# Kernel tuning notes

Measured on AMD Instinct MI355X. Metric: run time of the kernel, lower is better.

Reference implementation:

```python
import jax, jax.numpy as jnp
import numpy as np

T, B, C, H = 2048, 2, 1024, 16
DK = C // H


def setup_inputs() -> dict:
    key = jax.random.key(0)
    ks = jax.random.split(key, 12)
    s = 1.0 / np.sqrt(C)
    return {
        "query": jax.random.normal(ks[0], (T, B, C), jnp.float32),
        "key": jax.random.normal(ks[1], (T, B, C), jnp.float32),
        "value": jax.random.normal(ks[2], (T, B, C), jnp.float32),
        "Wq": jax.random.normal(ks[3], (C, C), jnp.float32) * s,
        "bq": jnp.zeros((C,), jnp.float32),
        "Wk": jax.random.normal(ks[4], (C, C), jnp.float32) * s,
        "bk": jnp.zeros((C,), jnp.float32),
        "Wv": jax.random.normal(ks[5], (C, C), jnp.float32) * s,
        "bv": jnp.zeros((C,), jnp.float32),
        "Wo": jax.random.normal(ks[6], (C, C), jnp.float32) * s,
        "bo": jnp.zeros((C,), jnp.float32),
        "key_padding_mask": jax.random.randint(ks[7], (B, T), 0, 2).astype(jnp.bool_),
    }


def reference(query, key, value, Wq, bq, Wk, bk, Wv, bv, Wo, bo, key_padding_mask):
    # T,B,C -> B,T,C
    q_in = jnp.transpose(query, (1, 0, 2))
    k_in = jnp.transpose(key, (1, 0, 2))
    v_in = jnp.transpose(value, (1, 0, 2))
    nb = q_in.shape[0]
    # linear projections, split heads: B,T,C -> B,H,T,dk
    def proj(x, W, b):
        y = x @ W.T + b
        return jnp.transpose(y.reshape(nb, -1, H, DK), (0, 2, 1, 3))
    q = proj(q_in, Wq, bq)
    k = proj(k_in, Wk, bk)
    v = proj(v_in, Wv, bv)
    # scores: B,H,T1,T2
    scores = jnp.einsum("bhqd,bhkd->bhqk", q, k) / np.sqrt(DK).astype(np.float32)
    scores = jnp.where(key_padding_mask[:, None, None, :], -jnp.inf, scores)
    attn = jax.nn.softmax(scores, axis=-1)
    # context: B,H,T1,dk -> B,T1,C
    x = jnp.einsum("bhqk,bhkd->bhqd", attn, v)
    x = jnp.transpose(x, (0, 2, 1, 3)).reshape(nb, -1, H * DK)
    out = x @ Wo.T + bo
    # B,T,C -> T,B,C
    return jnp.transpose(out, (1, 0, 2))
```

## Files before the change

### kernel.cpp

```cpp
#include <hip/hip_runtime.h>
#include <stdint.h>

typedef __attribute__((ext_vector_type(4))) float f32x4;
typedef __attribute__((ext_vector_type(8))) short bf16x8;
typedef __attribute__((ext_vector_type(2))) unsigned int u32x2;
typedef unsigned short u16;
typedef unsigned int u32;

#define DEVINL __device__ __forceinline__

DEVINL u16 f2bf(float f) {
  u32 u = __builtin_bit_cast(u32, f);
  u += 0x7FFFu + ((u >> 16) & 1u);
  return (u16)(u >> 16);
}

DEVINL float exp2_hw(float x) {
  float r;
  asm("v_exp_f32 %0, %1\n\ts_nop 0" : "=v"(r) : "v"(x));
  return r;
}

DEVINL u32 cvt_pk_bf16(float lo, float hi) {
  u32 r;
  asm("v_cvt_pk_bf16_f32 %0, %1, %2" : "=v"(r) : "v"(lo), "v"(hi));
  return r;
}

DEVINL void gload16(const void* g, void* l) {
  __builtin_amdgcn_global_load_lds((const __attribute__((address_space(1))) void*)g,
                                   (__attribute__((address_space(3))) void*)l, 16, 0, 0);
}

__global__ void cvt_all(const float* __restrict__ q, const float* __restrict__ k,
                        const float* __restrict__ v, const float* __restrict__ wq,
                        const float* __restrict__ wk, const float* __restrict__ wv,
                        const float* __restrict__ wo, ushort4* __restrict__ dst) {
  int i = blockIdx.x * 256 + threadIdx.x;
  float4 v4;
  if (i < 1048576) v4 = ((const float4*)q)[i];
  else if (i < 2097152) v4 = ((const float4*)k)[i - 1048576];
  else if (i < 3145728) v4 = ((const float4*)v)[i - 2097152];
  else {
    int j = i - 3145728;
    if (j < 262144) v4 = ((const float4*)wq)[j];
    else if (j < 524288) v4 = ((const float4*)wk)[j - 262144];
    else if (j < 786432) v4 = ((const float4*)wv)[j - 524288];
    else v4 = ((const float4*)wo)[j - 786432];
  }
  ushort4 o;
  o.x = f2bf(v4.x); o.y = f2bf(v4.y); o.z = f2bf(v4.z); o.w = f2bf(v4.w);
  dst[i] = o;
}

__global__ void mask_prep(const u32* __restrict__ mraw, float* __restrict__ mout) {
  __shared__ int notint, notfloat;
  int tid = threadIdx.x;
  if (tid == 0) { notint = 0; notfloat = 0; }
  __syncthreads();
  u32 w = mraw[tid];
  if (w != 0u && w != 1u) notint = 1;
  if (w != 0u && w != 0x3f800000u) notfloat = 1;
  __syncthreads();
  bool words = (!notint) || (!notfloat);
  for (int i = tid; i < 4096; i += 1024) {
    u32 v = words ? mraw[i] : (u32)(((const unsigned char*)mraw)[i]);
    mout[i] = v ? -1.0e38f : 0.0f;
  }
}

DEVINL void gemm_body(const u16* __restrict__ A, const u16* __restrict__ W,
                      const float* __restrict__ bias, u16* __restrict__ out_bf,
                      float* __restrict__ out_f, int tile, int mode,
                      u16* As, u16* Bs) {
  const int tid = threadIdx.x, lane = tid & 63;
  const int wave = tid >> 6, wm = wave & 1, wn = wave >> 1;
  const int m0 = (tile >> 3) << 7;
  const int n0 = (tile & 7) << 7;
  const int l15 = lane & 15, l4 = lane >> 4;
  const int K = 1024;
  const f32x4 zero = {0.f, 0.f, 0.f, 0.f};
  f32x4 acc[4][4];
#pragma unroll
  for (int i = 0; i < 4; i++)
#pragma unroll
    for (int j = 0; j < 4; j++) acc[i][j] = zero;

  for (int kt = 0; kt < 1024; kt += 32) {
#pragma unroll
    for (int it = 0; it < 2; ++it) {
      int c = tid + (it << 8);
      int row = c >> 2, qs = (c & 3) ^ ((row & 3) ^ ((row >> 2) & 3));
      gload16(A + (size_t)(m0 + row) * K + kt + qs * 8, (void*)(As + c * 8));
      gload16(W + (size_t)(n0 + row) * K + kt + qs * 8, (void*)(Bs + c * 8));
    }
    __syncthreads();
    bf16x8 af[4], bfr[4];
#pragma unroll
    for (int i = 0; i < 4; i++) {
      int ra = (wm << 6) + (i << 4) + l15;
      int rb = (wn << 6) + (i << 4) + l15;
      af[i]  = *(const bf16x8*)(As + ra * 32 + ((l4 * 8) ^ ((((ra & 3) ^ ((ra >> 2) & 3))) << 3)));
      bfr[i] = *(const bf16x8*)(Bs + rb * 32 + ((l4 * 8) ^ ((((rb & 3) ^ ((rb >> 2) & 3))) << 3)));
    }
#pragma unroll
    for (int i = 0; i < 4; i++)
#pragma unroll
      for (int j = 0; j < 4; j++)
        acc[i][j] = __builtin_amdgcn_mfma_f32_16x16x32_bf16(af[i], bfr[j], acc[i][j], 0, 0, 0);
    __syncthreads();
  }

#pragma unroll
  for (int j = 0; j < 4; j++) {
    const int col = n0 + (wn << 6) + (j << 4) + l15;
    const float bc = bias[col];
#pragma unroll
    for (int i = 0; i < 4; i++) {
#pragma unroll
      for (int r = 0; r < 4; r++) {
        const int row = m0 + (wm << 6) + (i << 4) + (l4 << 2) + r;
        float v = acc[i][j][r] + bc;
        if (mode == 3) {
          int t = row & 2047, b2 = row >> 11;
          out_f[(size_t)(t * 2 + b2) * 1024 + col] = v;
        } else {
          int t = row >> 1, b2 = row & 1, h = col >> 6, dh = col & 63;
          if (mode == 2)
            out_bf[((size_t)(b2 * 16 + h) * 64 + dh) * 2048 + t] = f2bf(v);
          else
            out_bf[((size_t)(b2 * 16 + h) * 2048 + t) * 64 + dh] = f2bf(v);
        }
      }
    }
  }
}

__global__ __launch_bounds__(256, 3) void gemm_qkv(
    const u16* __restrict__ qbf, const u16* __restrict__ kbf, const u16* __restrict__ vbf,
    const u16* __restrict__ wq, const u16* __restrict__ wk, const u16* __restrict__ wv,
    const float* __restrict__ bq, const float* __restrict__ bk, const float* __restrict__ bv,
    u16* __restrict__ Qh, u16* __restrict__ Kh, u16* __restrict__ Vth) {
  __shared__ u16 As[4096], Bs[4096];
  int wg = blockIdx.x;
  int swz = (wg & 7) * 96 + (wg >> 3);
  int prob = swz >> 8, tile = swz & 255;
  if (prob == 0)      gemm_body(qbf, wq, bq, Qh,  nullptr, tile, 0, As, Bs);
  else if (prob == 1) gemm_body(kbf, wk, bk, Kh,  nullptr, tile, 0, As, Bs);
  else                gemm_body(vbf, wv, bv, Vth, nullptr, tile, 2, As, Bs);
}

__global__ __launch_bounds__(256, 3) void gemm_o(
    const u16* __restrict__ ctx, const u16* __restrict__ wo,
    const float* __restrict__ bo, float* __restrict__ out) {
  __shared__ u16 As[4096], Bs[4096];
  int wg = blockIdx.x;
  int swz = (wg & 7) * 32 + (wg >> 3);
  gemm_body(ctx, wo, bo, nullptr, out, swz, 3, As, Bs);
}

__global__ __launch_bounds__(256, 4) void attn_fwd(
    const u16* __restrict__ Qh, const u16* __restrict__ Kh, const u16* __restrict__ Vt,
    const float* __restrict__ maskf, u16* __restrict__ ctx) {
  __shared__ u16 Ks[2][64 * 64];
  __shared__ u16 Vs[2][64 * 64];
  __shared__ u32 Plu[4][16 * 32];
  const int tid = threadIdx.x, lane = tid & 63, wave = tid >> 6;
  const int wg = blockIdx.x;
  const int swz = (wg & 7) * 128 + (wg >> 3);
  const int qt = swz & 31, bh = swz >> 5;
  const int bb = bh >> 4, h = bh & 15;
  const int l15 = lane & 15, l4 = lane >> 4;
  const f32x4 zero = {0.f, 0.f, 0.f, 0.f};
  const size_t kvbase = (size_t)bh * 2048 * 64;
  const float C2 = 0.18033688011112042f;

  bf16x8 qf[2];
#pragma unroll
  for (int kb = 0; kb < 2; kb++)
    qf[kb] = *(const bf16x8*)(Qh + kvbase + (size_t)(qt * 64 + wave * 16 + l15) * 64 + kb * 32 + l4 * 8);

  f32x4 O[4];
#pragma unroll
  for (int nd = 0; nd < 4; nd++) O[nd] = zero;
  float m_ = -1.0e30f, l_ = 0.f;

  auto stage = [&](int buf, int kt) {
#pragma unroll
    for (int it = 0; it < 2; ++it) {
      int c = tid + (it << 8);
      int row = c >> 3, qs = (c & 7) ^ (row & 7);
      gload16(Kh + kvbase + (size_t)(kt * 64 + row) * 64 + qs * 8, (void*)(&Ks[buf][c * 8]));
      gload16(Vt + kvbase + (size_t)row * 2048 + kt * 64 + qs * 8, (void*)(&Vs[buf][c * 8]));
    }
  };

  stage(0, 0);
  __syncthreads();

  const float4* mrow = (const float4*)(maskf + bb * 2048);

  for (int kt = 0; kt < 32; ++kt) {
    const int cur = kt & 1;
    if (kt < 31) stage(cur ^ 1, kt + 1);

    f32x4 s[4];
    __builtin_amdgcn_s_setprio(1);
#pragma unroll
    for (int ni = 0; ni < 4; ni++) {
      int row = ni * 16 + l15;
      s[ni] = zero;
#pragma unroll
      for (int kb = 0; kb < 2; kb++) {
        bf16x8 kf = *(const bf16x8*)(&Ks[cur][row * 64 + (((kb * 64 + l4 * 16) ^ ((row & 7) << 4)) >> 1)]);
        s[ni] = __builtin_amdgcn_mfma_f32_16x16x32_bf16(kf, qf[kb], s[ni], 0, 0, 0);
      }
    }
    __builtin_amdgcn_s_setprio(0);

#pragma unroll
    for (int ni = 0; ni < 4; ni++) {
      float4 mv = mrow[(kt * 16) + ni * 4 + l4];
      s[ni][0] = s[ni][0] * C2 + mv.x;
      s[ni][1] = s[ni][1] * C2 + mv.y;
      s[ni][2] = s[ni][2] * C2 + mv.z;
      s[ni][3] = s[ni][3] * C2 + mv.w;
    }

    float pm0 = fmaxf(fmaxf(s[0][0], s[0][1]), fmaxf(s[0][2], s[0][3]));
    float pm1 = fmaxf(fmaxf(s[1][0], s[1][1]), fmaxf(s[1][2], s[1][3]));
    float pm2 = fmaxf(fmaxf(s[2][0], s[2][1]), fmaxf(s[2][2], s[2][3]));
    float pm3 = fmaxf(fmaxf(s[3][0], s[3][1]), fmaxf(s[3][2], s[3][3]));
    float pm = fmaxf(fmaxf(pm0, pm1), fmaxf(pm2, pm3));
    pm = fmaxf(pm, __shfl_xor(pm, 16));
    pm = fmaxf(pm, __shfl_xor(pm, 32));

    if (__any(pm > m_ + 8.f)) {
      float mn = fmaxf(m_, pm);
      float al = exp2_hw(m_ - mn);
      m_ = mn;
      l_ *= al;
#pragma unroll
      for (int nd = 0; nd < 4; nd++)
#pragma unroll
        for (int r = 0; r < 4; r++) O[nd][r] *= al;
    }

    float rs = 0.f;
#pragma unroll
    for (int ni = 0; ni < 4; ni++) {
#pragma unroll
      for (int r = 0; r < 4; r++) {
        float p = exp2_hw(s[ni][r] - m_);
        s[ni][r] = p;
        rs += p;
      }
    }
    rs += __shfl_xor(rs, 16);
    rs += __shfl_xor(rs, 32);
    l_ += rs;

#pragma unroll
    for (int ni = 0; ni < 4; ni++) {
      u32x2 w;
      w.x = cvt_pk_bf16(s[ni][0], s[ni][1]);
      w.y = cvt_pk_bf16(s[ni][2], s[ni][3]);
      int col = ni * 8 + l4 * 2;
      *(u32x2*)(&Plu[wave][l15 * 32 + (col ^ ((l15 & 7) << 2))]) = w;
    }

    bf16x8 pb[2];
#pragma unroll
    for (int kb = 0; kb < 2; kb++) {
      int rcol = kb * 16 + l4 * 4;
      pb[kb] = *(const bf16x8*)(&Plu[wave][l15 * 32 + (rcol ^ ((l15 & 7) << 2))]);
    }
    __builtin_amdgcn_s_setprio(1);
#pragma unroll
    for (int nd = 0; nd < 4; nd++) {
      int row = nd * 16 + l15;
#pragma unroll
      for (int jb = 0; jb < 2; jb++) {
        bf16x8 vf = *(const bf16x8*)(&Vs[cur][row * 64 + (((jb * 64 + l4 * 16) ^ ((row & 7) << 4)) >> 1)]);
        O[nd] = __builtin_amdgcn_mfma_f32_16x16x32_bf16(vf, pb[jb], O[nd], 0, 0, 0);
      }
    }
    __builtin_amdgcn_s_setprio(0);

    __syncthreads();
  }

  float inv = (l_ > 0.f) ? 1.0f / l_ : 0.f;
  int t = qt * 64 + wave * 16 + l15;
  u16* cbase = ctx + ((size_t)bb * 2048 + t) * 1024 + h * 64;
#pragma unroll
  for (int nd = 0; nd < 4; nd++) {
    u32x2 w;
    w.x = cvt_pk_bf16(O[nd][0] * inv, O[nd][1] * inv);
    w.y = cvt_pk_bf16(O[nd][2] * inv, O[nd][3] * inv);
    *(u32x2*)(cbase + nd * 16 + l4 * 4) = w;
  }
}

extern "C" void kernel_launch(void* const* d_in, const int* in_sizes, int n_in,
                              void* d_out, int out_size, void* d_ws, size_t ws_size,
                              hipStream_t stream) {
  const float* q_in = (const float*)d_in[0];
  const float* k_in = (const float*)d_in[1];
  const float* v_in = (const float*)d_in[2];
  const float* Wq = (const float*)d_in[3];
  const float* bq = (const float*)d_in[4];
  const float* Wk = (const float*)d_in[5];
  const float* bk = (const float*)d_in[6];
  const float* Wv = (const float*)d_in[7];
  const float* bv = (const float*)d_in[8];
  const float* Wo = (const float*)d_in[9];
  const float* bo = (const float*)d_in[10];
  const void* mask = d_in[11];

  const size_t SZ_X = (size_t)4194304 * 2;
  const size_t SZ_W = (size_t)1048576 * 2;
  uint8_t* ws = (uint8_t*)d_ws;
  float* mf = (float*)ws;
  size_t off = 32768;
  u16* qbf = (u16*)(ws + off); off += SZ_X;
  u16* kbf = (u16*)(ws + off); off += SZ_X;
  u16* vbf = (u16*)(ws + off); off += SZ_X;
  u16* wqb = (u16*)(ws + off); off += SZ_W;
  u16* wkb = (u16*)(ws + off); off += SZ_W;
  u16* wvb = (u16*)(ws + off); off += SZ_W;
  u16* wob = (u16*)(ws + off); off += SZ_W;
  u16* Qh  = (u16*)(ws + off); off += SZ_X;
  u16* Kh  = (u16*)(ws + off); off += SZ_X;
  u16* Vth = (u16*)(ws + off); off += SZ_X;
  u16* ctx = (u16*)(ws + off); off += SZ_X;
  if (ws_size < off) return;

  mask_prep<<<1, 1024, 0, stream>>>((const u32*)mask, mf);
  cvt_all<<<16384, 256, 0, stream>>>(q_in, k_in, v_in, Wq, Wk, Wv, Wo, (ushort4*)qbf);

  gemm_qkv<<<768, 256, 0, stream>>>(qbf, kbf, vbf, wqb, wkb, wvb, bq, bk, bv, Qh, Kh, Vth);

  attn_fwd<<<1024, 256, 0, stream>>>(Qh, Kh, Vth, mf, ctx);

  gemm_o<<<256, 256, 0, stream>>>(ctx, wob, bo, (float*)d_out);
}
```

Measured before the change: 151.9 us.

## Switch attention to 32x32x16 MFMA with 128-query tiles and permlane P exchange

```diff
diff --git a/kernel.cpp b/kernel.cpp
--- a/kernel.cpp
+++ b/kernel.cpp
@@ -2,8 +2,10 @@
 #include <stdint.h>
 
 typedef __attribute__((ext_vector_type(4))) float f32x4;
+typedef __attribute__((ext_vector_type(16))) float f32x16;
 typedef __attribute__((ext_vector_type(8))) short bf16x8;
 typedef __attribute__((ext_vector_type(2))) unsigned int u32x2;
+typedef __attribute__((ext_vector_type(4))) unsigned int u32x4;
 typedef unsigned short u16;
 typedef unsigned int u32;
 
@@ -71,7 +73,7 @@
 
 DEVINL void gemm_body(const u16* __restrict__ A, const u16* __restrict__ W,
                       const float* __restrict__ bias, u16* __restrict__ out_bf,
-                      float* __restrict__ out_f, int tile, int mode,
+                      float* __restrict__ out_f, int tile, int mode, float scale,
                       u16* As, u16* Bs) {
   const int tid = threadIdx.x, lane = tid & 63;
   const int wave = tid >> 6, wm = wave & 1, wn = wave >> 1;
@@ -120,7 +122,7 @@
 #pragma unroll
       for (int r = 0; r < 4; r++) {
         const int row = m0 + (wm << 6) + (i << 4) + (l4 << 2) + r;
-        float v = acc[i][j][r] + bc;
+        float v = (acc[i][j][r] + bc) * scale;
         if (mode == 3) {
           int t = row & 2047, b2 = row >> 11;
           out_f[(size_t)(t * 2 + b2) * 1024 + col] = v;
@@ -142,12 +144,13 @@
     const float* __restrict__ bq, const float* __restrict__ bk, const float* __restrict__ bv,
     u16* __restrict__ Qh, u16* __restrict__ Kh, u16* __restrict__ Vth) {
   __shared__ u16 As[4096], Bs[4096];
+  const float C2 = 0.18033688011112042f;
   int wg = blockIdx.x;
   int swz = (wg & 7) * 96 + (wg >> 3);
   int prob = swz >> 8, tile = swz & 255;
-  if (prob == 0)      gemm_body(qbf, wq, bq, Qh,  nullptr, tile, 0, As, Bs);
-  else if (prob == 1) gemm_body(kbf, wk, bk, Kh,  nullptr, tile, 0, As, Bs);
-  else                gemm_body(vbf, wv, bv, Vth, nullptr, tile, 2, As, Bs);
+  if (prob == 0)      gemm_body(qbf, wq, bq, Qh,  nullptr, tile, 0, C2, As, Bs);
+  else if (prob == 1) gemm_body(kbf, wk, bk, Kh,  nullptr, tile, 0, 1.0f, As, Bs);
+  else                gemm_body(vbf, wv, bv, Vth, nullptr, tile, 2, 1.0f, As, Bs);
 }
 
 __global__ __launch_bounds__(256, 3) void gemm_o(
@@ -156,33 +159,33 @@
   __shared__ u16 As[4096], Bs[4096];
   int wg = blockIdx.x;
   int swz = (wg & 7) * 32 + (wg >> 3);
-  gemm_body(ctx, wo, bo, nullptr, out, swz, 3, As, Bs);
-}
-
-__global__ __launch_bounds__(256, 4) void attn_fwd(
+  gemm_body(ctx, wo, bo, nullptr, out, swz, 3, 1.0f, As, Bs);
+}
+
+__global__ __launch_bounds__(256, 2) void attn_fwd(
     const u16* __restrict__ Qh, const u16* __restrict__ Kh, const u16* __restrict__ Vt,
     const float* __restrict__ maskf, u16* __restrict__ ctx) {
   __shared__ u16 Ks[2][64 * 64];
   __shared__ u16 Vs[2][64 * 64];
-  __shared__ u32 Plu[4][16 * 32];
   const int tid = threadIdx.x, lane = tid & 63, wave = tid >> 6;
   const int wg = blockIdx.x;
-  const int swz = (wg & 7) * 128 + (wg >> 3);
-  const int qt = swz & 31, bh = swz >> 5;
+  const int swz = (wg & 7) * 64 + (wg >> 3);
+  const int qt = swz & 15, bh = swz >> 4;
   const int bb = bh >> 4, h = bh & 15;
-  const int l15 = lane & 15, l4 = lane >> 4;
-  const f32x4 zero = {0.f, 0.f, 0.f, 0.f};
+  const int l31 = lane & 31, hi = lane >> 5;
   const size_t kvbase = (size_t)bh * 2048 * 64;
-  const float C2 = 0.18033688011112042f;
-
-  bf16x8 qf[2];
-#pragma unroll
-  for (int kb = 0; kb < 2; kb++)
-    qf[kb] = *(const bf16x8*)(Qh + kvbase + (size_t)(qt * 64 + wave * 16 + l15) * 64 + kb * 32 + l4 * 8);
-
-  f32x4 O[4];
-#pragma unroll
-  for (int nd = 0; nd < 4; nd++) O[nd] = zero;
+  const int qbase = qt * 128 + wave * 32;
+
+  bf16x8 qf[4];
+#pragma unroll
+  for (int kc = 0; kc < 4; kc++)
+    qf[kc] = *(const bf16x8*)(Qh + kvbase + (size_t)(qbase + l31) * 64 + kc * 16 + hi * 8);
+
+  f32x16 zz;
+#pragma unroll
+  for (int e = 0; e < 16; e++) zz[e] = 0.f;
+  f32x16 O[2];
+  O[0] = zz; O[1] = zz;
   float m_ = -1.0e30f, l_ = 0.f;
 
   auto stage = [&](int buf, int kt) {
@@ -204,35 +207,35 @@
     const int cur = kt & 1;
     if (kt < 31) stage(cur ^ 1, kt + 1);
 
-    f32x4 s[4];
+    f32x16 s[2];
+    s[0] = zz; s[1] = zz;
     __builtin_amdgcn_s_setprio(1);
 #pragma unroll
-    for (int ni = 0; ni < 4; ni++) {
-      int row = ni * 16 + l15;
-      s[ni] = zero;
-#pragma unroll
-      for (int kb = 0; kb < 2; kb++) {
-        bf16x8 kf = *(const bf16x8*)(&Ks[cur][row * 64 + (((kb * 64 + l4 * 16) ^ ((row & 7) << 4)) >> 1)]);
-        s[ni] = __builtin_amdgcn_mfma_f32_16x16x32_bf16(kf, qf[kb], s[ni], 0, 0, 0);
+    for (int kc = 0; kc < 4; kc++) {
+      const int ch = (((kc * 2 + hi) ^ (l31 & 7)) << 3);
+      bf16x8 kf0 = *(const bf16x8*)(&Ks[cur][l31 * 64 + ch]);
+      bf16x8 kf1 = *(const bf16x8*)(&Ks[cur][(l31 + 32) * 64 + ch]);
+      s[0] = __builtin_amdgcn_mfma_f32_32x32x16_bf16(kf0, qf[kc], s[0], 0, 0, 0);
+      s[1] = __builtin_amdgcn_mfma_f32_32x32x16_bf16(kf1, qf[kc], s[1], 0, 0, 0);
+    }
+    __builtin_amdgcn_s_setprio(0);
+
+#pragma unroll
+    for (int kb = 0; kb < 2; kb++)
+#pragma unroll
+      for (int g = 0; g < 4; g++) {
+        float4 mv = mrow[kt * 16 + kb * 8 + g * 2 + hi];
+        s[kb][4 * g + 0] += mv.x;
+        s[kb][4 * g + 1] += mv.y;
+        s[kb][4 * g + 2] += mv.z;
+        s[kb][4 * g + 3] += mv.w;
       }
-    }
-    __builtin_amdgcn_s_setprio(0);
-
-#pragma unroll
-    for (int ni = 0; ni < 4; ni++) {
-      float4 mv = mrow[(kt * 16) + ni * 4 + l4];
-      s[ni][0] = s[ni][0] * C2 + mv.x;
-      s[ni][1] = s[ni][1] * C2 + mv.y;
-      s[ni][2] = s[ni][2] * C2 + mv.z;
-      s[ni][3] = s[ni][3] * C2 + mv.w;
-    }
-
-    float pm0 = fmaxf(fmaxf(s[0][0], s[0][1]), fmaxf(s[0][2], s[0][3]));
-    float pm1 = fmaxf(fmaxf(s[1][0], s[1][1]), fmaxf(s[1][2], s[1][3]));
-    float pm2 = fmaxf(fmaxf(s[2][0], s[2][1]), fmaxf(s[2][2], s[2][3]));
-    float pm3 = fmaxf(fmaxf(s[3][0], s[3][1]), fmaxf(s[3][2], s[3][3]));
-    float pm = fmaxf(fmaxf(pm0, pm1), fmaxf(pm2, pm3));
-    pm = fmaxf(pm, __shfl_xor(pm, 16));
+
+    float pm = s[0][0];
+#pragma unroll
+    for (int e = 1; e < 16; e++) pm = fmaxf(pm, s[0][e]);
+#pragma unroll
+    for (int e = 0; e < 16; e++) pm = fmaxf(pm, s[1][e]);
     pm = fmaxf(pm, __shfl_xor(pm, 32));
 
     if (__any(pm > m_ + 8.f)) {
@@ -241,65 +244,61 @@
       m_ = mn;
       l_ *= al;
 #pragma unroll
-      for (int nd = 0; nd < 4; nd++)
-#pragma unroll
-        for (int r = 0; r < 4; r++) O[nd][r] *= al;
+      for (int e = 0; e < 16; e++) { O[0][e] *= al; O[1][e] *= al; }
     }
 
     float rs = 0.f;
 #pragma unroll
-    for (int ni = 0; ni < 4; ni++) {
-#pragma unroll
-      for (int r = 0; r < 4; r++) {
-        float p = exp2_hw(s[ni][r] - m_);
-        s[ni][r] = p;
+    for (int kb = 0; kb < 2; kb++)
+#pragma unroll
+      for (int e = 0; e < 16; e++) {
+        float p = exp2_hw(s[kb][e] - m_);
+        s[kb][e] = p;
         rs += p;
       }
-    }
-    rs += __shfl_xor(rs, 16);
     rs += __shfl_xor(rs, 32);
     l_ += rs;
 
-#pragma unroll
-    for (int ni = 0; ni < 4; ni++) {
+    u32 pw[2][8];
+#pragma unroll
+    for (int kb = 0; kb < 2; kb++)
+#pragma unroll
+      for (int g = 0; g < 4; g++) {
+        pw[kb][2 * g]     = cvt_pk_bf16(s[kb][4 * g + 0], s[kb][4 * g + 1]);
+        pw[kb][2 * g + 1] = cvt_pk_bf16(s[kb][4 * g + 2], s[kb][4 * g + 3]);
+      }
+
+    __builtin_amdgcn_s_setprio(1);
+#pragma unroll
+    for (int kc = 0; kc < 4; kc++) {
+      const int kb = kc >> 1, m = kc & 1;
+      auto r0 = __builtin_amdgcn_permlane32_swap(pw[kb][4 * m + 0], pw[kb][4 * m + 2], false, false);
+      auto r1 = __builtin_amdgcn_permlane32_swap(pw[kb][4 * m + 1], pw[kb][4 * m + 3], false, false);
+      u32x4 fw = {r0[0], r1[0], r0[1], r1[1]};
+      bf16x8 pf = __builtin_bit_cast(bf16x8, fw);
+      const int ch = (((kc * 2 + hi) ^ (l31 & 7)) << 3);
+      bf16x8 vf0 = *(const bf16x8*)(&Vs[cur][l31 * 64 + ch]);
+      bf16x8 vf1 = *(const bf16x8*)(&Vs[cur][(l31 + 32) * 64 + ch]);
+      O[0] = __builtin_amdgcn_mfma_f32_32x32x16_bf16(vf0, pf, O[0], 0, 0, 0);
+      O[1] = __builtin_amdgcn_mfma_f32_32x32x16_bf16(vf1, pf, O[1], 0, 0, 0);
+    }
+    __builtin_amdgcn_s_setprio(0);
+
+    __syncthreads();
+  }
+
+  float inv = (l_ > 0.f) ? 1.0f / l_ : 0.f;
+  const int q = qbase + l31;
+  u16* cb = ctx + ((size_t)bb * 2048 + q) * 1024 + h * 64;
+#pragma unroll
+  for (int nd = 0; nd < 2; nd++)
+#pragma unroll
+    for (int g = 0; g < 4; g++) {
       u32x2 w;
-      w.x = cvt_pk_bf16(s[ni][0], s[ni][1]);
-      w.y = cvt_pk_bf16(s[ni][2], s[ni][3]);
-      int col = ni * 8 + l4 * 2;
-      *(u32x2*)(&Plu[wave][l15 * 32 + (col ^ ((l15 & 7) << 2))]) = w;
-    }
-
-    bf16x8 pb[2];
-#pragma unroll
-    for (int kb = 0; kb < 2; kb++) {
-      int rcol = kb * 16 + l4 * 4;
-      pb[kb] = *(const bf16x8*)(&Plu[wave][l15 * 32 + (rcol ^ ((l15 & 7) << 2))]);
-    }
-    __builtin_amdgcn_s_setprio(1);
-#pragma unroll
-    for (int nd = 0; nd < 4; nd++) {
-      int row = nd * 16 + l15;
-#pragma unroll
-      for (int jb = 0; jb < 2; jb++) {
-        bf16x8 vf = *(const bf16x8*)(&Vs[cur][row * 64 + (((jb * 64 + l4 * 16) ^ ((row & 7) << 4)) >> 1)]);
-        O[nd] = __builtin_amdgcn_mfma_f32_16x16x32_bf16(vf, pb[jb], O[nd], 0, 0, 0);
-      }
-    }
-    __builtin_amdgcn_s_setprio(0);
-
-    __syncthreads();
-  }
-
-  float inv = (l_ > 0.f) ? 1.0f / l_ : 0.f;
-  int t = qt * 64 + wave * 16 + l15;
-  u16* cbase = ctx + ((size_t)bb * 2048 + t) * 1024 + h * 64;
-#pragma unroll
-  for (int nd = 0; nd < 4; nd++) {
-    u32x2 w;
-    w.x = cvt_pk_bf16(O[nd][0] * inv, O[nd][1] * inv);
-    w.y = cvt_pk_bf16(O[nd][2] * inv, O[nd][3] * inv);
-    *(u32x2*)(cbase + nd * 16 + l4 * 4) = w;
-  }
+      w[0] = cvt_pk_bf16(O[nd][4 * g + 0] * inv, O[nd][4 * g + 1] * inv);
+      w[1] = cvt_pk_bf16(O[nd][4 * g + 2] * inv, O[nd][4 * g + 3] * inv);
+      *(u32x2*)(cb + nd * 32 + g * 8 + hi * 4) = w;
+    }
 }
 
 extern "C" void kernel_launch(void* const* d_in, const int* in_sizes, int n_in,
@@ -341,7 +340,7 @@
 
   gemm_qkv<<<768, 256, 0, stream>>>(qbf, kbf, vbf, wqb, wkb, wvb, bq, bk, bv, Qh, Kh, Vth);
 
-  attn_fwd<<<1024, 256, 0, stream>>>(Qh, Kh, Vth, mf, ctx);
+  attn_fwd<<<512, 256, 0, stream>>>(Qh, Kh, Vth, mf, ctx);
 
   gemm_o<<<256, 256, 0, stream>>>(ctx, wob, bo, (float*)d_out);
 }
```

Result: slower. 160.2 us (+5.4%).
